# Optimization experiments

Measured on AMD Instinct MI355X. Metric: run time of the kernel, lower is better.

The kernel has to match this reference:

```python
import jax, jax.numpy as jnp
import numpy as np


def setup_inputs() -> dict:
    key = jax.random.key(0)
    k1, k2, k3, k4 = jax.random.split(key, 4)
    B, S, E = 4, 2048, 2048
    x = jax.random.normal(k1, (B, S, E), dtype=jnp.float32)
    w_query = jax.random.normal(k2, (E, E), dtype=jnp.float32)
    w_key = jax.random.normal(k3, (E, E), dtype=jnp.float32)
    w_value = jax.random.normal(k4, (E, E), dtype=jnp.float32)
    return {"x": x, "w_query": w_query, "w_key": w_key, "w_value": w_value}


def reference(x, w_query, w_key, w_value):
    B, S, E = x.shape
    H = 16
    Dh = E // H  # query_size
    scale = 1.0 / jnp.sqrt(jnp.float32(Dh))
    # NOTE: original uses reshape (NOT transpose) from (B,S,H,Dh) -> (B,H,S,Dh),
    # a pure reinterpretation of the flat buffer. Replicate with direct reshape.
    q = (x @ w_query).reshape(B, H, S, Dh)
    k = (x @ w_key).reshape(B, H, S, Dh)
    v = (x @ w_value).reshape(B, H, S, Dh)
    scores = jnp.einsum("bhqd,bhkd->bhqk", q, k) * scale
    # original applies Softmax(dim=0) to each (S,S) score matrix -> query axis
    soft = jax.nn.softmax(scores, axis=2)
    attn = jnp.einsum("bhqk,bhkd->bhqd", soft, v)  # (B,H,S,Dh)
    # original: reshape (B,H,S,Dh)->(B,S,H,Dh)->(B,S,E), both pure reshapes
    return attn.reshape(B, S, E)
```

## Files before the change

### kernel.cpp

```cpp
#include <hip/hip_runtime.h>
#include <math.h>

typedef _Float16 half_t;
typedef __attribute__((ext_vector_type(8))) _Float16 f16x8;
typedef __attribute__((ext_vector_type(4))) _Float16 f16x4;
typedef __attribute__((ext_vector_type(4))) float f32x4;

#define MFMA __builtin_amdgcn_mfma_f32_16x16x32_f16
#define K1C (0.08838834764831845f * 1.4426950408889634f)
#define RLO (1.0f / 2048.0f)

__device__ inline void gld16(const void* g, void* l) {
  __builtin_amdgcn_global_load_lds(
      (const __attribute__((address_space(1))) uint32_t*)g,
      (__attribute__((address_space(3))) uint32_t*)l, 16, 0, 0);
}

__global__ __launch_bounds__(256) void split_x(const float* __restrict__ X,
                                               half_t* __restrict__ Xh,
                                               half_t* __restrict__ Xl) {
  size_t i = (size_t)blockIdx.x * 256 + threadIdx.x;
  const size_t stride = (size_t)gridDim.x * 256;
  for (size_t p = i; p < 4194304; p += stride) {
    f32x4 v = ((const f32x4*)X)[p];
    f16x4 h, l;
#pragma unroll
    for (int j = 0; j < 4; ++j) {
      half_t hh = (half_t)v[j];
      h[j] = hh;
      l[j] = (half_t)((v[j] - (float)hh) * 2048.0f);
    }
    ((f16x4*)Xh)[p] = h;
    ((f16x4*)Xl)[p] = l;
  }
}

__global__ __launch_bounds__(256) void wtrans_split(const float* __restrict__ W,
                                                    half_t* __restrict__ Wh,
                                                    half_t* __restrict__ Wl) {
  __shared__ float T[64][68];
  const int tid = threadIdx.x;
  const int k0 = blockIdx.x * 64, n0 = blockIdx.y * 64;
#pragma unroll
  for (int t = 0; t < 4; ++t) {
    int s = t * 256 + tid;
    int kr = s >> 4, nc = (s & 15) * 4;
    f32x4 v = *(const f32x4*)&W[(size_t)(k0 + kr) * 2048 + n0 + nc];
#pragma unroll
    for (int j = 0; j < 4; ++j) T[nc + j][kr] = v[j];
  }
  __syncthreads();
#pragma unroll
  for (int t = 0; t < 4; ++t) {
    int s = t * 256 + tid;
    int nr = s >> 4, kc = (s & 15) * 4;
    f16x4 h, l;
#pragma unroll
    for (int j = 0; j < 4; ++j) {
      float q = T[nr][kc + j];
      half_t hh = (half_t)q;
      h[j] = hh;
      l[j] = (half_t)((q - (float)hh) * 2048.0f);
    }
    *(f16x4*)&Wh[(size_t)(n0 + nr) * 2048 + k0 + kc] = h;
    *(f16x4*)&Wl[(size_t)(n0 + nr) * 2048 + k0 + kc] = l;
  }
}

__global__ __launch_bounds__(256, 2) void proj_mfma(
    const half_t* __restrict__ Xh, const half_t* __restrict__ Xl,
    const half_t* __restrict__ Wh, const half_t* __restrict__ Wl,
    half_t* __restrict__ Ch, half_t* __restrict__ Cl, const int mode) {
  __shared__ half_t sAh[4096], sAl[4096], sBh[4096], sBl[4096];
  const int tid = threadIdx.x;
  const int lid = blockIdx.x;
  const int swz = (lid & 7) * 128 + (lid >> 3);
  const int m0 = (swz >> 4) << 7, n0 = (swz & 15) << 7;
  const int w = tid >> 6, lane = tid & 63, c = lane & 15, g = lane >> 4;
  const int wr = w >> 1, wc = w & 1;
  f32x4 z4 = {0.f, 0.f, 0.f, 0.f};
  f32x4 acc0[4][4], accX[4][4];
#pragma unroll
  for (int i = 0; i < 4; ++i)
#pragma unroll
    for (int j = 0; j < 4; ++j) { acc0[i][j] = z4; accX[i][j] = z4; }
  for (int k0 = 0; k0 < 2048; k0 += 32) {
#pragma unroll
    for (int t = 0; t < 2; ++t) {
      int s = t * 256 + tid;
      int row = s >> 2;
      int lch = (s & 3) ^ ((row >> 1) & 3);
      size_t ga = (size_t)(m0 + row) * 2048 + k0 + lch * 8;
      size_t gb = (size_t)(n0 + row) * 2048 + k0 + lch * 8;
      gld16(&Xh[ga], &sAh[s * 8]);
      gld16(&Xl[ga], &sAl[s * 8]);
      gld16(&Wh[gb], &sBh[s * 8]);
      gld16(&Wl[gb], &sBl[s * 8]);
    }
    __syncthreads();
    {
      f16x8 a0[4], a1[4], b0[4], b1[4];
      const int sw = g ^ ((c >> 1) & 3);
#pragma unroll
      for (int i = 0; i < 4; ++i) {
        int ar = wr * 64 + i * 16 + c;
        a0[i] = *(const f16x8*)&sAh[ar * 32 + sw * 8];
        a1[i] = *(const f16x8*)&sAl[ar * 32 + sw * 8];
        int br = wc * 64 + i * 16 + c;
        b0[i] = *(const f16x8*)&sBh[br * 32 + sw * 8];
        b1[i] = *(const f16x8*)&sBl[br * 32 + sw * 8];
      }
#pragma unroll
      for (int i = 0; i < 4; ++i)
#pragma unroll
        for (int j = 0; j < 4; ++j) {
          acc0[i][j] = MFMA(a0[i], b0[j], acc0[i][j], 0, 0, 0);
          if (mode == 0) {
            accX[i][j] = MFMA(a0[i], b1[j], accX[i][j], 0, 0, 0);
            accX[i][j] = MFMA(a1[i], b0[j], accX[i][j], 0, 0, 0);
          }
        }
    }
    __syncthreads();
  }
#pragma unroll
  for (int i = 0; i < 4; ++i)
#pragma unroll
    for (int j = 0; j < 4; ++j) {
      int mbase = m0 + wr * 64 + i * 16 + g * 4;
      int n = n0 + wc * 64 + j * 16 + c;
#pragma unroll
      for (int r = 0; r < 4; ++r) {
        float q = acc0[i][j][r] + accX[i][j][r] * RLO;
        half_t hh = (half_t)q;
        size_t o = (size_t)(mbase + r) * 2048 + n;
        Ch[o] = hh;
        if (mode == 0) Cl[o] = (half_t)((q - (float)hh) * 2048.0f);
      }
    }
}

__global__ __launch_bounds__(256) void transpose_v(const half_t* __restrict__ V,
                                                   half_t* __restrict__ Vt) {
  __shared__ half_t T[128 * 128];
  const int tid = threadIdx.x;
  const int bh = blockIdx.y, k0 = blockIdx.x * 128;
  const size_t base = (size_t)bh << 18;
#pragma unroll
  for (int t = 0; t < 8; ++t) {
    int s = t * 256 + tid;
    int kr = s >> 4, ch = s & 15;
    int pc = ch ^ ((kr >> 3) & 15);
    *(f16x8*)&T[kr * 128 + pc * 8] =
        *(const f16x8*)&V[base + (size_t)(k0 + kr) * 128 + ch * 8];
  }
  __syncthreads();
#pragma unroll
  for (int t = 0; t < 8; ++t) {
    int s = t * 256 + tid;
    int d = s >> 4, kc = s & 15;
    f16x8 o;
#pragma unroll
    for (int j = 0; j < 8; ++j) {
      int kr = kc * 8 + j;
      int pc = (d >> 3) ^ (kc & 15);
      o[j] = T[kr * 128 + pc * 8 + (d & 7)];
    }
    *(f16x8*)&Vt[base + (size_t)d * 2048 + k0 + kc * 8] = o;
  }
}

#define STAGE_Q(nb, qn) do {                                                  \
    int r0_ = tid >> 4, cl0_ = tid & 15;                                      \
    size_t o0_ = base + (size_t)((qn) + r0_) * 128 + ((cl0_ ^ r0_) << 3);     \
    gld16(&Qh[o0_], &sQ0[nb][tid << 3]);                                      \
    gld16(&Ql[o0_], &sQ1[nb][tid << 3]);                                      \
    int r1_ = 16 + r0_;                                                       \
    size_t o1_ = base + (size_t)((qn) + r1_) * 128 + ((cl0_ ^ (r1_ & 15)) << 3); \
    gld16(&Qh[o1_], &sQ0[nb][(256 + tid) << 3]);                              \
    gld16(&Ql[o1_], &sQ1[nb][(256 + tid) << 3]);                              \
  } while (0)

__global__ __launch_bounds__(256) void stats_mfma(
    const half_t* __restrict__ Qh, const half_t* __restrict__ Ql,
    const half_t* __restrict__ Kh, const half_t* __restrict__ Kl,
    float* __restrict__ C2) {
  __shared__ half_t sQ0[2][4096], sQ1[2][4096];
  const int tid = threadIdx.x;
  const int w = tid >> 6, lane = tid & 63, c = lane & 15, g = lane >> 4;
  const int lid = blockIdx.y * 16 + blockIdx.x;
  const int bh = (lid & 7) * 8 + ((lid >> 3) & 7);
  const int xb = lid >> 6;
  const size_t base = (size_t)bh << 18;
  const int kb = xb * 128 + w * 32;
  f32x4 z4 = {0.f, 0.f, 0.f, 0.f};
  f16x8 ka0[2][4], ka1[2][4];
#pragma unroll
  for (int kt = 0; kt < 2; ++kt)
#pragma unroll
    for (int ds = 0; ds < 4; ++ds) {
      size_t a = base + (size_t)(kb + kt * 16 + c) * 128 + ds * 32 + g * 8;
      ka0[kt][ds] = *(const f16x8*)&Kh[a];
      ka1[kt][ds] = *(const f16x8*)&Kl[a];
    }
  float m[2][4], z[2][4];
#pragma unroll
  for (int kt = 0; kt < 2; ++kt)
#pragma unroll
    for (int r = 0; r < 4; ++r) { m[kt][r] = -INFINITY; z[kt][r] = 0.f; }
  STAGE_Q(0, 0);
  __syncthreads();
  for (int t = 0; t < 64; ++t) {
    const int buf = t & 1;
    if (t < 63) STAGE_Q(buf ^ 1, (t + 1) << 5);
#pragma unroll
    for (int qh = 0; qh < 2; ++qh) {
      f16x8 q0v[4], q1v[4];
#pragma unroll
      for (int ds = 0; ds < 4; ++ds) {
        int off = ((qh << 4) | c) * 128 + ((((ds << 2) | g) ^ c) << 3);
        q0v[ds] = *(const f16x8*)&sQ0[buf][off];
        q1v[ds] = *(const f16x8*)&sQ1[buf][off];
      }
#pragma unroll
      for (int kt = 0; kt < 2; ++kt) {
        f32x4 A0 = z4, AX = z4;
#pragma unroll
        for (int ds = 0; ds < 4; ++ds) {
          A0 = MFMA(ka0[kt][ds], q0v[ds], A0, 0, 0, 0);
          AX = MFMA(ka0[kt][ds], q1v[ds], AX, 0, 0, 0);
          AX = MFMA(ka1[kt][ds], q0v[ds], AX, 0, 0, 0);
        }
#pragma unroll
        for (int r = 0; r < 4; ++r) {
          float tt = (A0[r] + AX[r] * RLO) * K1C;
          float mo = m[kt][r];
          float mn = fmaxf(mo, tt);
          float e = __builtin_amdgcn_exp2f(fminf(mo, tt) - mn);
          z[kt][r] = (tt <= mo) ? (z[kt][r] + e) : (z[kt][r] * e + 1.0f);
          m[kt][r] = mn;
        }
      }
    }
    __syncthreads();
  }
#pragma unroll
  for (int mask = 1; mask < 16; mask <<= 1)
#pragma unroll
    for (int kt = 0; kt < 2; ++kt)
#pragma unroll
      for (int r = 0; r < 4; ++r) {
        float mo = __shfl_xor(m[kt][r], mask, 64);
        float zo = __shfl_xor(z[kt][r], mask, 64);
        float mn = fmaxf(m[kt][r], mo);
        z[kt][r] = z[kt][r] * __builtin_amdgcn_exp2f(m[kt][r] - mn) +
                   zo * __builtin_amdgcn_exp2f(mo - mn);
        m[kt][r] = mn;
      }
  if (c == 0) {
#pragma unroll
    for (int kt = 0; kt < 2; ++kt)
#pragma unroll
      for (int r = 0; r < 4; ++r)
        C2[(bh << 11) + kb + kt * 16 + (g << 2) + r] =
            m[kt][r] + __builtin_amdgcn_logf(z[kt][r]);
  }
}

#define STAGE_ATTN(nb, ktn) do {                                              \
    int r_ = tid >> 4, chl_ = tid & 15;                                       \
    size_t ro_ = base + (size_t)((ktn) + r_) * 128 + ((chl_ ^ (r_ & 15)) << 3); \
    gld16(&Kh[ro_], &sKh[nb][tid << 3]);                                      \
    gld16(&Kl[ro_], &sKl[nb][tid << 3]);                                      \
    int d_ = tid >> 2, cvl_ = tid & 3;                                        \
    gld16(&Vt[base + (size_t)d_ * 2048 + (ktn) + ((cvl_ ^ ((d_ >> 1) & 3)) << 3)], \
          &sVs[nb][tid << 3]);                                                \
  } while (0)

__global__ __launch_bounds__(512, 4) void attn_mfma(
    const half_t* __restrict__ Qh, const half_t* __restrict__ Ql,
    const half_t* __restrict__ Kh, const half_t* __restrict__ Kl,
    const half_t* __restrict__ Vt, const float* __restrict__ C2,
    float* __restrict__ O) {
  __shared__ half_t sKh[2][4096], sKl[2][4096], sVs[2][4096];
  __shared__ half_t sP[8][16][40];
  __shared__ float sC2[2048];
  const int tid = threadIdx.x;
  const int w = tid >> 6, lane = tid & 63, c = lane & 15, g = lane >> 4;
  const int lid = blockIdx.y * 16 + blockIdx.x;
  const int bh = (lid & 7) * 8 + ((lid >> 3) & 7);
  const int qx = lid >> 6;
  const size_t base = (size_t)bh << 18;
  const int qb = qx * 128 + w * 16;
  f32x4 z4 = {0.f, 0.f, 0.f, 0.f};
  f16x8 qf0[4], qf1[4];
#pragma unroll
  for (int ds = 0; ds < 4; ++ds) {
    size_t a = base + (size_t)(qb + c) * 128 + ds * 32 + g * 8;
    qf0[ds] = *(const f16x8*)&Qh[a];
    qf1[ds] = *(const f16x8*)&Ql[a];
  }
  f32x4 Oacc[8];
#pragma unroll
  for (int dt = 0; dt < 8; ++dt) Oacc[dt] = z4;
  ((f32x4*)sC2)[tid] = ((const f32x4*)(C2 + ((size_t)bh << 11)))[tid];
  STAGE_ATTN(0, 0);
  __syncthreads();
  for (int t = 0; t < 64; ++t) {
    const int buf = t & 1;
    const int kt = t << 5;
    if (t < 63) STAGE_ATTN(buf ^ 1, kt + 32);
#pragma unroll
    for (int h = 0; h < 2; ++h) {
      f32x4 A0 = z4, AX = z4;
#pragma unroll
      for (int ds = 0; ds < 4; ++ds) {
        int off = ((h << 4) | c) * 128 + ((((ds << 2) | g) ^ c) << 3);
        f16x8 k0v = *(const f16x8*)&sKh[buf][off];
        f16x8 k1v = *(const f16x8*)&sKl[buf][off];
        A0 = MFMA(k0v, qf0[ds], A0, 0, 0, 0);
        AX = MFMA(k0v, qf1[ds], AX, 0, 0, 0);
        AX = MFMA(k1v, qf0[ds], AX, 0, 0, 0);
      }
      f32x4 c2v = *(const f32x4*)&sC2[kt + (h << 4) + (g << 2)];
      f16x4 pv;
#pragma unroll
      for (int r = 0; r < 4; ++r)
        pv[r] = (half_t)__builtin_amdgcn_exp2f((A0[r] + AX[r] * RLO) * K1C - c2v[r]);
      *(f16x4*)&sP[w][c][(h << 4) + (g << 2)] = pv;
    }
    f16x8 pa = *(const f16x8*)&sP[w][c][g << 3];
#pragma unroll
    for (int dt = 0; dt < 8; ++dt) {
      int dd = (dt << 4) + c;
      f16x8 vb = *(const f16x8*)&sVs[buf][dd * 32 + ((g ^ ((dd >> 1) & 3)) << 3)];
      Oacc[dt] = MFMA(pa, vb, Oacc[dt], 0, 0, 0);
    }
    __syncthreads();
  }
#pragma unroll
  for (int dt = 0; dt < 8; ++dt)
#pragma unroll
    for (int r = 0; r < 4; ++r)
      O[base + (size_t)(qb + (g << 2) + r) * 128 + (dt << 4) + c] = Oacc[dt][r];
}

extern "C" void kernel_launch(void* const* d_in, const int* in_sizes, int n_in,
                              void* d_out, int out_size, void* d_ws, size_t ws_size,
                              hipStream_t stream) {
  (void)in_sizes; (void)n_in; (void)out_size; (void)ws_size;
  const float* x = (const float*)d_in[0];
  const float* wq = (const float*)d_in[1];
  const float* wk = (const float*)d_in[2];
  const float* wv = (const float*)d_in[3];
  float* out = (float*)d_out;
  char* ws = (char*)d_ws;
  const size_t S2 = 33554432;
  half_t* Wth = (half_t*)ws;
  half_t* Wtl = (half_t*)(ws + 8388608);
  half_t* Qh = (half_t*)(ws + 16777216);
  half_t* Ql = (half_t*)(ws + 16777216 + S2);
  half_t* Kh = (half_t*)(ws + 16777216 + 2 * S2);
  half_t* Kl = (half_t*)(ws + 16777216 + 3 * S2);
  half_t* Vh = (half_t*)(ws + 16777216 + 4 * S2);
  half_t* Vth = (half_t*)(ws + 16777216 + 5 * S2);
  float* C2 = (float*)(ws + 16777216 + 6 * S2);
  half_t* Xh = (half_t*)d_out;
  half_t* Xl = (half_t*)((char*)d_out + S2);
  dim3 b(256);
  split_x<<<2048, b, 0, stream>>>(x, Xh, Xl);
  wtrans_split<<<dim3(32, 32), b, 0, stream>>>(wq, Wth, Wtl);
  proj_mfma<<<dim3(1024), b, 0, stream>>>(Xh, Xl, Wth, Wtl, Qh, Ql, 0);
  wtrans_split<<<dim3(32, 32), b, 0, stream>>>(wk, Wth, Wtl);
  proj_mfma<<<dim3(1024), b, 0, stream>>>(Xh, Xl, Wth, Wtl, Kh, Kl, 0);
  wtrans_split<<<dim3(32, 32), b, 0, stream>>>(wv, Wth, Wtl);
  proj_mfma<<<dim3(1024), b, 0, stream>>>(Xh, Xl, Wth, Wtl, Vh, nullptr, 1);
  transpose_v<<<dim3(16, 64), b, 0, stream>>>(Vh, Vth);
  stats_mfma<<<dim3(16, 64), b, 0, stream>>>(Qh, Ql, Kh, Kl, C2);
  attn_mfma<<<dim3(16, 64), dim3(512), 0, stream>>>(Qh, Ql, Kh, Kl, Vth, C2, out);
}
```

Before: 1.114 ms.

## Double-buffer projection GEMM loads and widen stats kernel key tile per block

The projection GEMM now stages the next K-slice into a second LDS buffer while MFMAs run on the current one. This is meant to overlap global-to-LDS loads with compute instead of serialising them behind a barrier. The stats kernel now gives each warp 64 keys instead of 32 and launches half as many blocks, which halves how often Q tiles are re-streamed. The costs are doubled LDS use in proj (64KB per block) and more VGPRs for K fragments and softmax state in stats, both of which can lower occupancy.

```diff
diff --git a/kernel.cpp b/kernel.cpp
--- a/kernel.cpp
+++ b/kernel.cpp
@@ -67,11 +67,26 @@
   }
 }
 
+#define STAGE_P(nb, kn) do {                                                  \
+    _Pragma("unroll")                                                         \
+    for (int t_ = 0; t_ < 2; ++t_) {                                          \
+      int s_ = t_ * 256 + tid;                                                \
+      int row_ = s_ >> 2;                                                     \
+      int lch_ = (s_ & 3) ^ ((row_ >> 1) & 3);       \
+      size_t ga_ = (size_t)(m0 + row_) * 2048 + (kn) + lch_ * 8;              \
+      size_t gb_ = (size_t)(n0 + row_) * 2048 + (kn) + lch_ * 8;              \
+      gld16(&Xh[ga_], &sAh[nb][s_ * 8]);                                      \
+      gld16(&Xl[ga_], &sAl[nb][s_ * 8]);                                      \
+      gld16(&Wh[gb_], &sBh[nb][s_ * 8]);                                      \
+      gld16(&Wl[gb_], &sBl[nb][s_ * 8]);                                      \
+    }                                                                         \
+  } while (0)
+
 __global__ __launch_bounds__(256, 2) void proj_mfma(
     const half_t* __restrict__ Xh, const half_t* __restrict__ Xl,
     const half_t* __restrict__ Wh, const half_t* __restrict__ Wl,
     half_t* __restrict__ Ch, half_t* __restrict__ Cl, const int mode) {
-  __shared__ half_t sAh[4096], sAl[4096], sBh[4096], sBl[4096];
+  __shared__ half_t sAh[2][4096], sAl[2][4096], sBh[2][4096], sBl[2][4096];
   const int tid = threadIdx.x;
   const int lid = blockIdx.x;
   const int swz = (lid & 7) * 128 + (lid >> 3);
@@ -84,31 +99,22 @@
   for (int i = 0; i < 4; ++i)
 #pragma unroll
     for (int j = 0; j < 4; ++j) { acc0[i][j] = z4; accX[i][j] = z4; }
+  STAGE_P(0, 0);
+  __syncthreads();
   for (int k0 = 0; k0 < 2048; k0 += 32) {
-#pragma unroll
-    for (int t = 0; t < 2; ++t) {
-      int s = t * 256 + tid;
-      int row = s >> 2;
-      int lch = (s & 3) ^ ((row >> 1) & 3);
-      size_t ga = (size_t)(m0 + row) * 2048 + k0 + lch * 8;
-      size_t gb = (size_t)(n0 + row) * 2048 + k0 + lch * 8;
-      gld16(&Xh[ga], &sAh[s * 8]);
-      gld16(&Xl[ga], &sAl[s * 8]);
-      gld16(&Wh[gb], &sBh[s * 8]);
-      gld16(&Wl[gb], &sBl[s * 8]);
-    }
-    __syncthreads();
+    const int buf = (k0 >> 5) & 1;
+    if (k0 < 2016) STAGE_P(buf ^ 1, k0 + 32);
     {
       f16x8 a0[4], a1[4], b0[4], b1[4];
       const int sw = g ^ ((c >> 1) & 3);
 #pragma unroll
       for (int i = 0; i < 4; ++i) {
         int ar = wr * 64 + i * 16 + c;
-        a0[i] = *(const f16x8*)&sAh[ar * 32 + sw * 8];
-        a1[i] = *(const f16x8*)&sAl[ar * 32 + sw * 8];
+        a0[i] = *(const f16x8*)&sAh[buf][ar * 32 + sw * 8];
+        a1[i] = *(const f16x8*)&sAl[buf][ar * 32 + sw * 8];
         int br = wc * 64 + i * 16 + c;
-        b0[i] = *(const f16x8*)&sBh[br * 32 + sw * 8];
-        b1[i] = *(const f16x8*)&sBl[br * 32 + sw * 8];
+        b0[i] = *(const f16x8*)&sBh[buf][br * 32 + sw * 8];
+        b1[i] = *(const f16x8*)&sBl[buf][br * 32 + sw * 8];
       }
 #pragma unroll
       for (int i = 0; i < 4; ++i)
@@ -181,31 +187,31 @@
     gld16(&Ql[o1_], &sQ1[nb][(256 + tid) << 3]);                              \
   } while (0)
 
-__global__ __launch_bounds__(256) void stats_mfma(
+__global__ __launch_bounds__(256, 2) void stats_mfma(
     const half_t* __restrict__ Qh, const half_t* __restrict__ Ql,
     const half_t* __restrict__ Kh, const half_t* __restrict__ Kl,
     float* __restrict__ C2) {
   __shared__ half_t sQ0[2][4096], sQ1[2][4096];
   const int tid = threadIdx.x;
   const int w = tid >> 6, lane = tid & 63, c = lane & 15, g = lane >> 4;
-  const int lid = blockIdx.y * 16 + blockIdx.x;
+  const int lid = blockIdx.y * 8 + blockIdx.x;
   const int bh = (lid & 7) * 8 + ((lid >> 3) & 7);
   const int xb = lid >> 6;
   const size_t base = (size_t)bh << 18;
-  const int kb = xb * 128 + w * 32;
+  const int kb = xb * 256 + w * 64;
   f32x4 z4 = {0.f, 0.f, 0.f, 0.f};
-  f16x8 ka0[2][4], ka1[2][4];
-#pragma unroll
-  for (int kt = 0; kt < 2; ++kt)
+  f16x8 ka0[4][4], ka1[4][4];
+#pragma unroll
+  for (int kt = 0; kt < 4; ++kt)
 #pragma unroll
     for (int ds = 0; ds < 4; ++ds) {
       size_t a = base + (size_t)(kb + kt * 16 + c) * 128 + ds * 32 + g * 8;
       ka0[kt][ds] = *(const f16x8*)&Kh[a];
       ka1[kt][ds] = *(const f16x8*)&Kl[a];
     }
-  float m[2][4], z[2][4];
-#pragma unroll
-  for (int kt = 0; kt < 2; ++kt)
+  float m[4][4], z[4][4];
+#pragma unroll
+  for (int kt = 0; kt < 4; ++kt)
 #pragma unroll
     for (int r = 0; r < 4; ++r) { m[kt][r] = -INFINITY; z[kt][r] = 0.f; }
   STAGE_Q(0, 0);
@@ -223,7 +229,7 @@
         q1v[ds] = *(const f16x8*)&sQ1[buf][off];
       }
 #pragma unroll
-      for (int kt = 0; kt < 2; ++kt) {
+      for (int kt = 0; kt < 4; ++kt) {
         f32x4 A0 = z4, AX = z4;
 #pragma unroll
         for (int ds = 0; ds < 4; ++ds) {
@@ -247,7 +253,7 @@
 #pragma unroll
   for (int mask = 1; mask < 16; mask <<= 1)
 #pragma unroll
-    for (int kt = 0; kt < 2; ++kt)
+    for (int kt = 0; kt < 4; ++kt)
 #pragma unroll
       for (int r = 0; r < 4; ++r) {
         float mo = __shfl_xor(m[kt][r], mask, 64);
@@ -259,7 +265,7 @@
       }
   if (c == 0) {
 #pragma unroll
-    for (int kt = 0; kt < 2; ++kt)
+    for (int kt = 0; kt < 4; ++kt)
 #pragma unroll
       for (int r = 0; r < 4; ++r)
         C2[(bh << 11) + kb + kt * 16 + (g << 2) + r] =
@@ -376,6 +382,6 @@
   wtrans_split<<<dim3(32, 32), b, 0, stream>>>(wv, Wth, Wtl);
   proj_mfma<<<dim3(1024), b, 0, stream>>>(Xh, Xl, Wth, Wtl, Vh, nullptr, 1);
   transpose_v<<<dim3(16, 64), b, 0, stream>>>(Vh, Vth);
-  stats_mfma<<<dim3(16, 64), b, 0, stream>>>(Qh, Ql, Kh, Kl, C2);
+  stats_mfma<<<dim3(8, 64), b, 0, stream>>>(Qh, Ql, Kh, Kl, C2);
   attn_mfma<<<dim3(16, 64), dim3(512), 0, stream>>>(Qh, Ql, Kh, Kl, Vth, C2, out);
 }
```

Result: faster. 1.085 ms (-2.6%).
